# Optimization experiments

Measured on AMD Instinct MI355X. Metric: run time of the kernel, lower is better.

The kernel has to match this reference:

```python
import jax, jax.numpy as jnp
import numpy as np

B, T, D, H = 2, 1024, 1024, 16
DH = D // H
_PAIRS = [(0, 1), (0, 2), (0, 3), (1, 2), (1, 3), (2, 3)]
_J6 = jnp.array([[0, 0, 0, 0, 0, 1],
                 [0, 0, 0, 0, -1, 0],
                 [0, 0, 0, 1, 0, 0],
                 [0, 0, 1, 0, 0, 0],
                 [0, -1, 0, 0, 0, 0],
                 [1, 0, 0, 0, 0, 0]], dtype=jnp.float32)


def exterior(p1, p2):
    # Plucker coordinates of the line through 4-vectors p1, p2, L2-normalized.
    parts = [p1[..., i] * p2[..., j] - p1[..., j] * p2[..., i] for i, j in _PAIRS]
    L = jnp.stack(parts, axis=-1)  # (..., 6)
    n = jnp.maximum(jnp.linalg.norm(L, axis=-1, keepdims=True), 1e-12)
    return L / n


def setup_inputs() -> dict:
    key = jax.random.key(0)
    ks = jax.random.split(key, 10)
    s = 0.02
    return {
        "x": jax.random.normal(ks[0], (B, T, D), jnp.float32),
        "Wqkv": jax.random.normal(ks[1], (3 * D, D), jnp.float32) * s,
        "bqkv": jnp.zeros((3 * D,), jnp.float32),
        "W1w": jax.random.normal(ks[2], (4 * H, D), jnp.float32) * s,
        "W2w": jax.random.normal(ks[3], (4 * H, D), jnp.float32) * s,
        "W1r": jax.random.normal(ks[4], (4 * H, D), jnp.float32) * s,
        "W2r": jax.random.normal(ks[5], (4 * H, D), jnp.float32) * s,
        "bias_scale": jnp.full((H,), 0.1, jnp.float32),
        "Wout": jax.random.normal(ks[6], (D, D), jnp.float32) * s,
        "bout": jnp.zeros((D,), jnp.float32),
    }


def reference(x, Wqkv, bqkv, W1w, W2w, W1r, W2r, bias_scale, Wout, bout):
    Bb, Tt, Dd = x.shape
    scale = DH ** (-0.5)
    qkv = (x @ Wqkv.T + bqkv).reshape(Bb, Tt, 3, H, DH)
    q = jnp.transpose(qkv[:, :, 0], (0, 2, 1, 3))  # (B,H,T,dh)
    k = jnp.transpose(qkv[:, :, 1], (0, 2, 1, 3))
    v = jnp.transpose(qkv[:, :, 2], (0, 2, 1, 3))
    std_logits = jnp.einsum('bhtd,bhsd->bhts', q, k) * scale

    x_prev = jnp.concatenate([jnp.zeros((Bb, 1, Dd), x.dtype), x[:, :-1]], axis=1)
    w1 = (x_prev @ W1w.T).reshape(Bb, Tt, H, 4)
    w2 = (x @ W2w.T).reshape(Bb, Tt, H, 4)
    write_lines = exterior(w1, w2)  # (B,T,H,6)
    r1 = (x @ W1r.T).reshape(Bb, Tt, H, 4)
    r2 = (x @ W2r.T).reshape(Bb, Tt, H, 4)
    read_lines = exterior(r1, r2)  # (B,T,H,6)

    Jw = jnp.einsum('bthi,ij->bhtj', write_lines, _J6)  # (B,H,T,6)
    rd = jnp.transpose(read_lines, (0, 2, 1, 3))        # (B,H,T,6)

    outer = Jw[..., :, None] * Jw[..., None, :]          # (B,H,T,6,6)
    M_causal = jnp.cumsum(outer, axis=2)                 # running Gram state
    rd_M = jnp.einsum('bhti,bhtij->bhtj', rd, M_causal)  # (B,H,T,6)
    bias_raw = jnp.einsum('bhti,bhsi->bhts', rd_M, Jw)   # (B,H,T,T)
    bias = jnp.abs(bias_raw) * bias_scale.reshape(1, H, 1, 1)

    logits = std_logits + bias
    mask = jnp.triu(jnp.ones((Tt, Tt), bool), 1)
    logits = jnp.where(mask, -jnp.inf, logits)
    attn = jax.nn.softmax(logits, axis=-1)
    out = jnp.einsum('bhts,bhsd->bthd', attn, v).reshape(Bb, Tt, Dd)
    return out @ Wout.T + bout
```

## Files before the change

kernel.cpp:

```cpp
#include <hip/hip_runtime.h>
#include <math.h>

#define B_ 2
#define T_ 1024
#define D_ 1024
#define H_ 16
#define NA_ 3328

typedef __attribute__((ext_vector_type(8))) short bf16x8;
typedef __attribute__((ext_vector_type(4))) float f32x4;

__device__ inline unsigned short f2bf(float x) {
  return (unsigned short)((__float_as_uint(x) + 0x8000u) >> 16);
}
__device__ inline unsigned bfpack(float lo, float hi) {
  unsigned a = __float_as_uint(hi) + 0x8000u;
  unsigned b = __float_as_uint(lo) + 0x8000u;
  return __builtin_amdgcn_perm(a, b, 0x07060302);
}
__device__ inline void hl_split(float x, unsigned short& h, unsigned short& l) {
  unsigned short hh = f2bf(x);
  float hf = __uint_as_float(((unsigned)hh) << 16);
  l = f2bf(x - hf);
  h = hh;
}


#define GEMM_PROLOGUE_VARS()                                                   \
  const int tid = threadIdx.x;                                                 \
  const int w = tid >> 6, lane = tid & 63;                                     \
  const int lr = lane & 15, g = lane >> 4;                                     \
  const int wm = (w >> 1) * 64, wn = (w & 1) * 64;                             \
  const int row = tid >> 1, half = tid & 1;                                    \
  const int sw = (row & 3) << 4;                                               \
  const int by0 = (half * 32) ^ sw, by1 = (half * 32 + 16) ^ sw;

#define GEMM_STORE(bufA, bufB, a, b)                                           \
  {                                                                            \
    uint4 lo = make_uint4(bfpack(a[0].x, a[0].y), bfpack(a[0].z, a[0].w),      \
                          bfpack(a[1].x, a[1].y), bfpack(a[1].z, a[1].w));     \
    uint4 hi = make_uint4(bfpack(a[2].x, a[2].y), bfpack(a[2].z, a[2].w),      \
                          bfpack(a[3].x, a[3].y), bfpack(a[3].z, a[3].w));     \
    *(uint4*)(bufA + row * 64 + by0) = lo;                                     \
    *(uint4*)(bufA + row * 64 + by1) = hi;                                     \
    lo = make_uint4(bfpack(b[0].x, b[0].y), bfpack(b[0].z, b[0].w),            \
                    bfpack(b[1].x, b[1].y), bfpack(b[1].z, b[1].w));           \
    hi = make_uint4(bfpack(b[2].x, b[2].y), bfpack(b[2].z, b[2].w),            \
                    bfpack(b[3].x, b[3].y), bfpack(b[3].z, b[3].w));           \
    *(uint4*)(bufB + row * 64 + by0) = lo;                                     \
    *(uint4*)(bufB + row * 64 + by1) = hi;                                     \
  }

#define GEMM_COMPUTE(bufA, bufB)                                               \
  {                                                                            \
    bf16x8 af[4], bfr[4];                                                      \
    _Pragma("unroll") for (int i = 0; i < 4; ++i) {                            \
      const int rr = wm + i * 16 + lr;                                         \
      af[i] = *(const bf16x8*)(bufA + rr * 64 + ((g * 16) ^ ((rr & 3) << 4))); \
    }                                                                          \
    _Pragma("unroll") for (int i = 0; i < 4; ++i) {                            \
      const int rr = wn + i * 16 + lr;                                         \
      bfr[i] = *(const bf16x8*)(bufB + rr * 64 + ((g * 16) ^ ((rr & 3) << 4)));\
    }                                                                          \
    _Pragma("unroll") for (int i = 0; i < 4; ++i)                              \
    _Pragma("unroll") for (int j = 0; j < 4; ++j)                              \
      acc[i][j] = __builtin_amdgcn_mfma_f32_16x16x32_bf16(af[i], bfr[j],       \
                                                          acc[i][j], 0, 0, 0); \
  }

#define GEMM_LOAD(dst, base, slab)                                             \
  _Pragma("unroll") for (int i = 0; i < 4; ++i)                                \
      dst[i] = *(const float4*)(base + (slab) * 32 + i * 4);

__global__ __launch_bounds__(256) void gemm_qkv(
    const float* __restrict__ A, const float* __restrict__ Wqkv,
    const float* __restrict__ bqkv,
    const float* __restrict__ W1w, const float* __restrict__ W2w,
    const float* __restrict__ W1r, const float* __restrict__ W2r,
    float* __restrict__ C)
{
  __shared__ __align__(16) unsigned char As[2 * 8192];
  __shared__ __align__(16) unsigned char Bs[2 * 8192];
  const int m0 = blockIdx.y * 128, n0 = blockIdx.x * 128;
  GEMM_PROLOGUE_VARS();

  const float* Ap = A + (size_t)(m0 + row) * D_ + half * 16;
  const float* Bp;
  {
    const int cg = n0 + row;
    if (cg < 3072) Bp = Wqkv + (size_t)cg * D_;
    else {
      const int r = cg - 3072;
      const float* Wm = (r < 64) ? W1w : (r < 128) ? W2w : (r < 192) ? W1r : W2r;
      Bp = Wm + (size_t)(r & 63) * D_;
    }
    Bp += half * 16;
  }

  f32x4 acc[4][4];
  const f32x4 zf = {0.f, 0.f, 0.f, 0.f};
#pragma unroll
  for (int i = 0; i < 4; ++i)
#pragma unroll
    for (int j = 0; j < 4; ++j) acc[i][j] = zf;

  float4 aA[4], bA[4], aB[4], bB[4];
  GEMM_LOAD(aA, Ap, 0); GEMM_LOAD(bA, Bp, 0);
  GEMM_STORE(As, Bs, aA, bA);
  GEMM_LOAD(aB, Ap, 1); GEMM_LOAD(bB, Bp, 1);
  __syncthreads();

#pragma unroll 1
  for (int s = 0; s < 32; s += 2) {
    GEMM_COMPUTE(As, Bs);
    GEMM_STORE((As + 8192), (Bs + 8192), aB, bB);
    if (s + 2 < 32) { GEMM_LOAD(aA, Ap, s + 2); GEMM_LOAD(bA, Bp, s + 2); }
    __syncthreads();
    GEMM_COMPUTE((As + 8192), (Bs + 8192));
    if (s + 2 < 32) GEMM_STORE(As, Bs, aA, bA);
    if (s + 3 < 32) { GEMM_LOAD(aB, Ap, s + 3); GEMM_LOAD(bB, Bp, s + 3); }
    __syncthreads();
  }

#pragma unroll
  for (int i = 0; i < 4; ++i) {
    const int rbase = m0 + wm + i * 16 + 4 * g;
#pragma unroll
    for (int j = 0; j < 4; ++j) {
      const int col = n0 + wn + j * 16 + lr;
      const float bb = (col < 3072) ? bqkv[col] : 0.f;
#pragma unroll
      for (int r = 0; r < 4; ++r)
        C[(size_t)(rbase + r) * NA_ + col] = acc[i][j][r] + bb;
    }
  }
}

__global__ __launch_bounds__(256) void gemm_out(
    const float* __restrict__ A, const float* __restrict__ Bm,
    const float* __restrict__ bias, float* __restrict__ C)
{
  __shared__ __align__(16) unsigned char As[2 * 8192];
  __shared__ __align__(16) unsigned char Bs[2 * 8192];
  const int m0 = blockIdx.y * 128, n0 = blockIdx.x * 128;
  GEMM_PROLOGUE_VARS();

  const float* Ap = A + (size_t)(m0 + row) * D_ + half * 16;
  const float* Bp = Bm + (size_t)(n0 + row) * D_ + half * 16;

  f32x4 acc[4][4];
  const f32x4 zf = {0.f, 0.f, 0.f, 0.f};
#pragma unroll
  for (int i = 0; i < 4; ++i)
#pragma unroll
    for (int j = 0; j < 4; ++j) acc[i][j] = zf;

  float4 aA[4], bA[4], aB[4], bB[4];
  GEMM_LOAD(aA, Ap, 0); GEMM_LOAD(bA, Bp, 0);
  GEMM_STORE(As, Bs, aA, bA);
  GEMM_LOAD(aB, Ap, 1); GEMM_LOAD(bB, Bp, 1);
  __syncthreads();

#pragma unroll 1
  for (int s = 0; s < 32; s += 2) {
    GEMM_COMPUTE(As, Bs);
    GEMM_STORE((As + 8192), (Bs + 8192), aB, bB);
    if (s + 2 < 32) { GEMM_LOAD(aA, Ap, s + 2); GEMM_LOAD(bA, Bp, s + 2); }
    __syncthreads();
    GEMM_COMPUTE((As + 8192), (Bs + 8192));
    if (s + 2 < 32) GEMM_STORE(As, Bs, aA, bA);
    if (s + 3 < 32) { GEMM_LOAD(aB, Ap, s + 3); GEMM_LOAD(bB, Bp, s + 3); }
    __syncthreads();
  }

#pragma unroll
  for (int i = 0; i < 4; ++i) {
    const int rbase = m0 + wm + i * 16 + 4 * g;
#pragma unroll
    for (int j = 0; j < 4; ++j) {
      const int col = n0 + wn + j * 16 + lr;
      const float bb = bias[col];
#pragma unroll
      for (int r = 0; r < 4; ++r)
        C[(size_t)(rbase + r) * D_ + col] = acc[i][j][r] + bb;
    }
  }
}

__global__ __launch_bounds__(256) void exterior_kernel(
    const float* __restrict__ qkvp,
    float* __restrict__ Jw, float* __restrict__ rd,
    unsigned* __restrict__ Jwpk)
{
  const int i = blockIdx.x * 256 + threadIdx.x;
  const int h = i & 15;
  const int t = (i >> 4) & 1023;
  const int b = i >> 14;
  const size_t rowt = ((size_t)(b * T_) + t) * NA_;

  float4 p1w = make_float4(0.f, 0.f, 0.f, 0.f);
  if (t > 0) p1w = *(const float4*)(qkvp + rowt - NA_ + 3072 + h * 4);
  const float4 p2w = *(const float4*)(qkvp + rowt + 3136 + h * 4);
  const float4 p1r = *(const float4*)(qkvp + rowt + 3200 + h * 4);
  const float4 p2r = *(const float4*)(qkvp + rowt + 3264 + h * 4);

  const size_t base = ((size_t)(b * H_ + h) * T_ + t) * 6;
  {
    const float L0 = p1w.x * p2w.y - p1w.y * p2w.x;
    const float L1 = p1w.x * p2w.z - p1w.z * p2w.x;
    const float L2 = p1w.x * p2w.w - p1w.w * p2w.x;
    const float L3 = p1w.y * p2w.z - p1w.z * p2w.y;
    const float L4 = p1w.y * p2w.w - p1w.w * p2w.y;
    const float L5 = p1w.z * p2w.w - p1w.w * p2w.z;
    const float n = sqrtf(L0 * L0 + L1 * L1 + L2 * L2 + L3 * L3 + L4 * L4 + L5 * L5);
    const float inv = 1.f / fmaxf(n, 1e-12f);
    float jv[6] = {L5 * inv, -L4 * inv, L3 * inv, L2 * inv, -L1 * inv, L0 * inv};
#pragma unroll
    for (int k = 0; k < 6; ++k) Jw[base + k] = jv[k];
    unsigned short JH[6], JL[6];
#pragma unroll
    for (int k = 0; k < 6; ++k) hl_split(jv[k], JH[k], JL[k]);
    unsigned* jp = Jwpk + (((size_t)(b * H_ + h) * T_ + t) << 4);
    unsigned h01 = JH[0] | ((unsigned)JH[1] << 16);
    unsigned h23 = JH[2] | ((unsigned)JH[3] << 16);
    unsigned h45 = JH[4] | ((unsigned)JH[5] << 16);
    jp[0] = h01; jp[1] = h23; jp[2] = h45;
    jp[3] = JL[0] | ((unsigned)JL[1] << 16);
    jp[4] = JL[2] | ((unsigned)JL[3] << 16);
    jp[5] = JL[4] | ((unsigned)JL[5] << 16);
    jp[6] = h01; jp[7] = h23; jp[8] = h45;
#pragma unroll
    for (int k = 9; k < 16; ++k) jp[k] = 0;
  }
  {
    const float L0 = p1r.x * p2r.y - p1r.y * p2r.x;
    const float L1 = p1r.x * p2r.z - p1r.z * p2r.x;
    const float L2 = p1r.x * p2r.w - p1r.w * p2r.x;
    const float L3 = p1r.y * p2r.z - p1r.z * p2r.y;
    const float L4 = p1r.y * p2r.w - p1r.w * p2r.y;
    const float L5 = p1r.z * p2r.w - p1r.w * p2r.z;
    const float n = sqrtf(L0 * L0 + L1 * L1 + L2 * L2 + L3 * L3 + L4 * L4 + L5 * L5);
    const float inv = 1.f / fmaxf(n, 1e-12f);
    rd[base + 0] = L0 * inv;
    rd[base + 1] = L1 * inv;
    rd[base + 2] = L2 * inv;
    rd[base + 3] = L3 * inv;
    rd[base + 4] = L4 * inv;
    rd[base + 5] = L5 * inv;
  }
}

__global__ __launch_bounds__(256) void scan_kernel(
    const float* __restrict__ Jw, const float* __restrict__ rd,
    unsigned* __restrict__ rdMpk)
{
  __shared__ float sc[256][36];
  const int tid = threadIdx.x;
  const int bh = blockIdx.x;
  const float* Jb = Jw + (size_t)bh * T_ * 6;
  const float* Rb = rd + (size_t)bh * T_ * 6;
  const int t0 = tid * 4;

  float M[36];
#pragma unroll
  for (int i = 0; i < 36; ++i) M[i] = 0.f;
  for (int tt = 0; tt < 4; ++tt) {
    float j6[6];
#pragma unroll
    for (int i = 0; i < 6; ++i) j6[i] = Jb[(size_t)(t0 + tt) * 6 + i];
#pragma unroll
    for (int a = 0; a < 6; ++a)
#pragma unroll
      for (int c = 0; c < 6; ++c)
        M[a * 6 + c] = fmaf(j6[a], j6[c], M[a * 6 + c]);
  }
#pragma unroll
  for (int i = 0; i < 36; ++i) sc[tid][i] = M[i];
  __syncthreads();

  float Mp[36];
#pragma unroll
  for (int i = 0; i < 36; ++i) Mp[i] = 0.f;
  for (int j = 0; j < tid; ++j) {
#pragma unroll
    for (int i = 0; i < 36; ++i) Mp[i] += sc[j][i];
  }

  for (int tt = 0; tt < 4; ++tt) {
    const int t = t0 + tt;
    float j6[6], r6[6];
#pragma unroll
    for (int i = 0; i < 6; ++i) { j6[i] = Jb[(size_t)t * 6 + i]; r6[i] = Rb[(size_t)t * 6 + i]; }
#pragma unroll
    for (int a = 0; a < 6; ++a)
#pragma unroll
      for (int c = 0; c < 6; ++c)
        Mp[a * 6 + c] = fmaf(j6[a], j6[c], Mp[a * 6 + c]);
    float s6[6];
#pragma unroll
    for (int jj = 0; jj < 6; ++jj) {
      float s = 0.f;
#pragma unroll
      for (int a = 0; a < 6; ++a) s = fmaf(r6[a], Mp[a * 6 + jj], s);
      s6[jj] = s;
    }
    unsigned short hh[6], ll[6];
#pragma unroll
    for (int i = 0; i < 6; ++i) hl_split(s6[i], hh[i], ll[i]);
    unsigned* ob = rdMpk + (((size_t)bh * T_ + t) << 4);
    unsigned h01 = hh[0] | ((unsigned)hh[1] << 16);
    unsigned h23 = hh[2] | ((unsigned)hh[3] << 16);
    unsigned h45 = hh[4] | ((unsigned)hh[5] << 16);
    ob[0] = h01; ob[1] = h23; ob[2] = h45;
    ob[3] = h01; ob[4] = h23; ob[5] = h45;
    ob[6] = ll[0] | ((unsigned)ll[1] << 16);
    ob[7] = ll[2] | ((unsigned)ll[3] << 16);
    ob[8] = ll[4] | ((unsigned)ll[5] << 16);
#pragma unroll
    for (int i = 9; i < 16; ++i) ob[i] = 0;
  }
}

__global__ __launch_bounds__(256) void attn_mfma(
    const float* __restrict__ qkv,
    const unsigned* __restrict__ Jwpk,
    const unsigned* __restrict__ rdMpk,
    const float* __restrict__ bias_scale,
    float* __restrict__ attnout)
{
  __shared__ __align__(16) unsigned char smem[31744];
  unsigned char* KT = smem;
  unsigned char* VT = smem + 9216;
  unsigned*      JW = (unsigned*)(smem + 18432);
  unsigned char* PB = smem + 22528;

  const int gid = blockIdx.x;
  const int bh = gid & 31;
  const int c = (gid < 256) ? (15 - (gid >> 5)) : ((gid - 256) >> 5);
  const int b = bh >> 4, h = bh & 15;
  const int tid = threadIdx.x;
  const int w = tid >> 6;
  const int lane = tid & 63;
  const int lr = lane & 15;
  const int g = lane >> 4;
  const int t0 = c * 64;
  const int nT = c + 1;

  const size_t qkvbase = ((size_t)b * T_) * NA_ + h * 64;
  const size_t jb = (size_t)(b * H_ + h) * T_;

  int srow[4], scol[4];
#pragma unroll
  for (int p = 0; p < 4; ++p) {
    const int idx = p * 256 + tid;
    srow[p] = idx >> 4;
    scol[p] = (idx & 15) * 4;
  }

#pragma unroll
  for (int p = 0; p < 4; ++p) {
    const float4 v = *(const float4*)(qkv + qkvbase + (size_t)(t0 + srow[p]) * NA_ + scol[p]);
    const unsigned d0 = bfpack(v.x * 0.125f, v.y * 0.125f);
    const unsigned d1 = bfpack(v.z * 0.125f, v.w * 0.125f);
    const int byte = srow[p] * 144 + ((scol[p] * 2) ^ ((srow[p] & 7) << 4));
    *(uint2*)(KT + byte) = make_uint2(d0, d1);
  }
  __syncthreads();
  bf16x8 qa[2];
  {
    const int qrow = w * 16 + lr;
#pragma unroll
    for (int kb = 0; kb < 2; ++kb) {
      const int byte = qrow * 144 + (((kb * 64) + 16 * g) ^ ((qrow & 7) << 4));
      qa[kb] = *(const bf16x8*)(KT + byte);
    }
  }
  bf16x8 ra;
  {
    const int t = t0 + w * 16 + lr;
    ra = *(const bf16x8*)(rdMpk + ((jb + t) << 4) + g * 4);
  }
  const float bsc = bias_scale[h];
  __syncthreads();

  float m[4], lsum[4];
  f32x4 O[4];
  const f32x4 zf = {0.f, 0.f, 0.f, 0.f};
#pragma unroll
  for (int r = 0; r < 4; ++r) { m[r] = -1e30f; lsum[r] = 0.f; }
#pragma unroll
  for (int d = 0; d < 4; ++d) O[d] = zf;

  float4 kreg[4], vreg[4];
  uint4 jreg;
  const int jrow = tid >> 2, jpart = (tid & 3) * 4;
  {
#pragma unroll
    for (int p = 0; p < 4; ++p) {
      const size_t rb = qkvbase + (size_t)srow[p] * NA_ + scol[p];
      kreg[p] = *(const float4*)(qkv + rb + 1024);
      vreg[p] = *(const float4*)(qkv + rb + 2048);
    }
    jreg = *(const uint4*)(Jwpk + ((jb + jrow) << 4) + jpart);
  }

  for (int ti = 0; ti < nT; ++ti) {
    const int s0 = ti * 64;
    __syncthreads();
#pragma unroll
    for (int p = 0; p < 4; ++p) {
      const unsigned d0 = bfpack(kreg[p].x, kreg[p].y);
      const unsigned d1 = bfpack(kreg[p].z, kreg[p].w);
      const int byte = srow[p] * 144 + ((scol[p] * 2) ^ ((srow[p] & 7) << 4));
      *(uint2*)(KT + byte) = make_uint2(d0, d1);
      const int s = srow[p];
#pragma unroll
      for (int i = 0; i < 4; ++i) {
        const int d = scol[p] + i;
        const float vv = (i == 0) ? vreg[p].x : (i == 1) ? vreg[p].y : (i == 2) ? vreg[p].z : vreg[p].w;
        const int vbyte = d * 144 + ((2 * s) ^ ((d & 7) << 4));
        *(unsigned short*)(VT + vbyte) = f2bf(vv);
      }
    }
    *(uint4*)(JW + jrow * 16 + jpart) = jreg;
    __syncthreads();
    if (ti + 1 < nT) {
      const int s0n = s0 + 64;
#pragma unroll
      for (int p = 0; p < 4; ++p) {
        const size_t rb = qkvbase + (size_t)(s0n + srow[p]) * NA_ + scol[p];
        kreg[p] = *(const float4*)(qkv + rb + 1024);
        vreg[p] = *(const float4*)(qkv + rb + 2048);
      }
      jreg = *(const uint4*)(Jwpk + ((jb + s0n + jrow) << 4) + jpart);
    }

    f32x4 S[4], Sb[4];
#pragma unroll
    for (int cb = 0; cb < 4; ++cb) {
      const int srw = cb * 16 + lr;
      f32x4 a = zf;
#pragma unroll
      for (int kb = 0; kb < 2; ++kb) {
        const int byte = srw * 144 + (((kb * 64) + 16 * g) ^ ((srw & 7) << 4));
        const bf16x8 kf = *(const bf16x8*)(KT + byte);
        a = __builtin_amdgcn_mfma_f32_16x16x32_bf16(qa[kb], kf, a, 0, 0, 0);
      }
      S[cb] = a;
      union { uint4 u; bf16x8 v; } tmp;
      tmp.u = *(const uint4*)(JW + srw * 16 + g * 4);
      Sb[cb] = __builtin_amdgcn_mfma_f32_16x16x32_bf16(ra, tmp.v, zf, 0, 0, 0);
    }

    const bool diag = (s0 == t0);
    float logit[4][4];
#pragma unroll
    for (int cb = 0; cb < 4; ++cb) {
#pragma unroll
      for (int r = 0; r < 4; ++r) {
        float lg = S[cb][r] + fabsf(Sb[cb][r]) * bsc;
        if (diag && (cb * 16 + lr > w * 16 + 4 * g + r)) lg = -1e30f;
        logit[cb][r] = lg;
      }
    }
#pragma unroll
    for (int r = 0; r < 4; ++r) {
      float mx = fmaxf(fmaxf(logit[0][r], logit[1][r]), fmaxf(logit[2][r], logit[3][r]));
      mx = fmaxf(mx, __shfl_xor(mx, 1));
      mx = fmaxf(mx, __shfl_xor(mx, 2));
      mx = fmaxf(mx, __shfl_xor(mx, 4));
      mx = fmaxf(mx, __shfl_xor(mx, 8));
      const float nm = fmaxf(m[r], mx);
      const float sc = __expf(m[r] - nm);
      m[r] = nm;
      lsum[r] *= sc;
#pragma unroll
      for (int d = 0; d < 4; ++d) O[d][r] *= sc;
    }
#pragma unroll
    for (int cb = 0; cb < 4; ++cb) {
#pragma unroll
      for (int r = 0; r < 4; ++r) {
        const float p = __expf(logit[cb][r] - m[r]);
        lsum[r] += p;
        const int q = 4 * g + r;
        const int s = cb * 16 + lr;
        const int byte = w * 2304 + q * 144 + ((2 * s) ^ ((q & 7) << 4));
        *(unsigned short*)(PB + byte) = f2bf(p);
      }
    }
    asm volatile("s_waitcnt lgkmcnt(0)" ::: "memory");
    __builtin_amdgcn_sched_barrier(0);

    bf16x8 pa[2];
#pragma unroll
    for (int kb = 0; kb < 2; ++kb) {
      const int byte = w * 2304 + lr * 144 + (((kb * 64) + 16 * g) ^ ((lr & 7) << 4));
      pa[kb] = *(const bf16x8*)(PB + byte);
    }
#pragma unroll
    for (int db = 0; db < 4; ++db) {
#pragma unroll
      for (int kb = 0; kb < 2; ++kb) {
        const int d = db * 16 + lr;
        const int byte = d * 144 + (((kb * 64) + 16 * g) ^ ((d & 7) << 4));
        const bf16x8 vf = *(const bf16x8*)(VT + byte);
        O[db] = __builtin_amdgcn_mfma_f32_16x16x32_bf16(pa[kb], vf, O[db], 0, 0, 0);
      }
    }
  }

#pragma unroll
  for (int r = 0; r < 4; ++r) {
    float l = lsum[r];
    l += __shfl_xor(l, 1);
    l += __shfl_xor(l, 2);
    l += __shfl_xor(l, 4);
    l += __shfl_xor(l, 8);
    lsum[r] = 1.f / l;
  }
  {
    const int qb = w * 16 + 4 * g;
#pragma unroll
    for (int db = 0; db < 4; ++db) {
#pragma unroll
      for (int r = 0; r < 4; ++r) {
        const int t = t0 + qb + r;
        attnout[((size_t)(b * T_ + t)) * 1024 + h * 64 + db * 16 + lr] = O[db][r] * lsum[r];
      }
    }
  }
}

extern "C" void kernel_launch(void* const* d_in, const int* in_sizes, int n_in,
                              void* d_out, int out_size, void* d_ws, size_t ws_size,
                              hipStream_t stream)
{
  (void)in_sizes; (void)n_in; (void)out_size; (void)ws_size;
  const float* x    = (const float*)d_in[0];
  const float* Wqkv = (const float*)d_in[1];
  const float* bqkv = (const float*)d_in[2];
  const float* W1w  = (const float*)d_in[3];
  const float* W2w  = (const float*)d_in[4];
  const float* W1r  = (const float*)d_in[5];
  const float* W2r  = (const float*)d_in[6];
  const float* bsc  = (const float*)d_in[7];
  const float* Wout = (const float*)d_in[8];
  const float* bout = (const float*)d_in[9];
  float* out = (float*)d_out;

  float*    qkvp    = (float*)d_ws;
  float*    Jw      = qkvp + (size_t)B_ * T_ * NA_;
  float*    rd      = Jw + (size_t)B_ * H_ * T_ * 6;
  unsigned* Jwpk    = (unsigned*)(rd + (size_t)B_ * H_ * T_ * 6);
  unsigned* rdMpk   = Jwpk + ((size_t)B_ * H_ * T_ << 4);
  float*    attnout = (float*)(rdMpk + ((size_t)B_ * H_ * T_ << 4));

  gemm_qkv<<<dim3(NA_ / 128, B_ * T_ / 128), 256, 0, stream>>>(
      x, Wqkv, bqkv, W1w, W2w, W1r, W2r, qkvp);
  exterior_kernel<<<dim3(B_ * T_ * H_ / 256), 256, 0, stream>>>(
      qkvp, Jw, rd, Jwpk);
  scan_kernel<<<dim3(B_ * H_), 256, 0, stream>>>(Jw, rd, rdMpk);
  attn_mfma<<<dim3(B_ * H_ * (T_ / 64)), 256, 0, stream>>>(
      qkvp, Jwpk, rdMpk, bsc, attnout);
  gemm_out<<<dim3(D_ / 128, B_ * T_ / 128), 256, 0, stream>>>(
      attnout, Wout, bout, out);
}
```

Measured before the change: 139.9 us.

## Pre-convert inputs to bf16, store QKV and attention output in bf16, parallel scan

Adds a kernel that converts x and all weight matrices to bf16 once, so the GEMMs load bf16 tiles directly instead of converting fp32 in the inner loop. The GEMMs switch to 128x64 tiles with 128 threads and a swizzled block order. QKV and the attention output are now written as bf16, and the projection lines go to a separate fp32 buffer. The attention kernel reads Q and K fragments straight from global bf16 and double-buffers a transposed V tile. The scan kernel replaces its serial prefix loop with a Hillis-Steele scan in shared memory. Per-call weight conversion adds extra traffic, and keeping intermediates in bf16 lowers precision.

```diff
diff --git a/kernel.cpp b/kernel.cpp
--- a/kernel.cpp
+++ b/kernel.cpp
@@ -5,7 +5,6 @@
 #define T_ 1024
 #define D_ 1024
 #define H_ 16
-#define NA_ 3328
 
 typedef __attribute__((ext_vector_type(8))) short bf16x8;
 typedef __attribute__((ext_vector_type(4))) float f32x4;
@@ -25,170 +24,164 @@
   h = hh;
 }
 
-
-#define GEMM_PROLOGUE_VARS()                                                   \
+#define CN1 2097152
+#define CN2 3407872
+#define CN3 1048576
+__global__ __launch_bounds__(256) void convert_kernel(
+    const float* __restrict__ x, const float* __restrict__ Wqkv,
+    const float* __restrict__ W1w, const float* __restrict__ W2w,
+    const float* __restrict__ W1r, const float* __restrict__ W2r,
+    const float* __restrict__ Wout,
+    unsigned short* __restrict__ xb, unsigned short* __restrict__ Wb,
+    unsigned short* __restrict__ Woutb)
+{
+  const long i8 = ((long)blockIdx.x * 256 + threadIdx.x) * 8;
+  const float* src;
+  unsigned short* dst;
+  if (i8 < CN1) {
+    src = x + i8; dst = xb + i8;
+  } else if (i8 < CN1 + CN2) {
+    const long j = i8 - CN1;
+    const int row = (int)(j >> 10), col = (int)(j & 1023);
+    if (row < 3072) src = Wqkv + (size_t)row * 1024 + col;
+    else {
+      const int r = row - 3072;
+      const float* Wm = (r < 64) ? W1w : (r < 128) ? W2w : (r < 192) ? W1r : W2r;
+      src = Wm + (size_t)(r & 63) * 1024 + col;
+    }
+    dst = Wb + j;
+  } else {
+    const long j = i8 - CN1 - CN2;
+    src = Wout + j; dst = Woutb + j;
+  }
+  const float4 v0 = *(const float4*)src;
+  const float4 v1 = *(const float4*)(src + 4);
+  uint4 o;
+  o.x = bfpack(v0.x, v0.y); o.y = bfpack(v0.z, v0.w);
+  o.z = bfpack(v1.x, v1.y); o.w = bfpack(v1.z, v1.w);
+  *(uint4*)dst = o;
+}
+
+#define G_PRO()                                                                \
   const int tid = threadIdx.x;                                                 \
   const int w = tid >> 6, lane = tid & 63;                                     \
   const int lr = lane & 15, g = lane >> 4;                                     \
-  const int wm = (w >> 1) * 64, wn = (w & 1) * 64;                             \
-  const int row = tid >> 1, half = tid & 1;                                    \
-  const int sw = (row & 3) << 4;                                               \
-  const int by0 = (half * 32) ^ sw, by1 = (half * 32 + 16) ^ sw;
-
-#define GEMM_STORE(bufA, bufB, a, b)                                           \
-  {                                                                            \
-    uint4 lo = make_uint4(bfpack(a[0].x, a[0].y), bfpack(a[0].z, a[0].w),      \
-                          bfpack(a[1].x, a[1].y), bfpack(a[1].z, a[1].w));     \
-    uint4 hi = make_uint4(bfpack(a[2].x, a[2].y), bfpack(a[2].z, a[2].w),      \
-                          bfpack(a[3].x, a[3].y), bfpack(a[3].z, a[3].w));     \
-    *(uint4*)(bufA + row * 64 + by0) = lo;                                     \
-    *(uint4*)(bufA + row * 64 + by1) = hi;                                     \
-    lo = make_uint4(bfpack(b[0].x, b[0].y), bfpack(b[0].z, b[0].w),            \
-                    bfpack(b[1].x, b[1].y), bfpack(b[1].z, b[1].w));           \
-    hi = make_uint4(bfpack(b[2].x, b[2].y), bfpack(b[2].z, b[2].w),            \
-                    bfpack(b[3].x, b[3].y), bfpack(b[3].z, b[3].w));           \
-    *(uint4*)(bufB + row * 64 + by0) = lo;                                     \
-    *(uint4*)(bufB + row * 64 + by1) = hi;                                     \
-  }
-
-#define GEMM_COMPUTE(bufA, bufB)                                               \
-  {                                                                            \
-    bf16x8 af[4], bfr[4];                                                      \
-    _Pragma("unroll") for (int i = 0; i < 4; ++i) {                            \
-      const int rr = wm + i * 16 + lr;                                         \
-      af[i] = *(const bf16x8*)(bufA + rr * 64 + ((g * 16) ^ ((rr & 3) << 4))); \
-    }                                                                          \
-    _Pragma("unroll") for (int i = 0; i < 4; ++i) {                            \
-      const int rr = wn + i * 16 + lr;                                         \
-      bfr[i] = *(const bf16x8*)(bufB + rr * 64 + ((g * 16) ^ ((rr & 3) << 4)));\
-    }                                                                          \
-    _Pragma("unroll") for (int i = 0; i < 4; ++i)                              \
-    _Pragma("unroll") for (int j = 0; j < 4; ++j)                              \
-      acc[i][j] = __builtin_amdgcn_mfma_f32_16x16x32_bf16(af[i], bfr[j],       \
-                                                          acc[i][j], 0, 0, 0); \
-  }
-
-#define GEMM_LOAD(dst, base, slab)                                             \
+  const int wm = w * 64;                                                       \
+  const int brow = tid & 63, bhalf = tid >> 6;
+
+#define G_LOADA(d, s) {                                                        \
+  d[0] = *(const uint4*)(Ap + (s) * 32);                                       \
+  d[1] = *(const uint4*)(Ap + (s) * 32 + 8);                                   \
+  d[2] = *(const uint4*)(Ap + (s) * 32 + 16);                                  \
+  d[3] = *(const uint4*)(Ap + (s) * 32 + 24); }
+#define G_LOADB(d, s) {                                                        \
+  d[0] = *(const uint4*)(Bp + (s) * 32);                                       \
+  d[1] = *(const uint4*)(Bp + (s) * 32 + 8); }
+#define G_STORE(bi, a, b) {                                                    \
+  unsigned char* SA_ = As + (bi) * 8192;                                       \
+  *(uint4*)(SA_ + 0 * 2048 + tid * 16) = a[0];                                 \
+  *(uint4*)(SA_ + 1 * 2048 + tid * 16) = a[1];                                 \
+  *(uint4*)(SA_ + 2 * 2048 + tid * 16) = a[2];                                 \
+  *(uint4*)(SA_ + 3 * 2048 + tid * 16) = a[3];                                 \
+  unsigned char* SB_ = Bs + (bi) * 4096;                                       \
+  *(uint4*)(SB_ + (2 * bhalf) * 1024 + brow * 16) = b[0];                      \
+  *(uint4*)(SB_ + (2 * bhalf + 1) * 1024 + brow * 16) = b[1]; }
+#define G_COMPUTE(bi) {                                                        \
+  const unsigned char* SA_ = As + (bi) * 8192;                                 \
+  const unsigned char* SB_ = Bs + (bi) * 4096;                                 \
+  bf16x8 af[4], bfr[4];                                                        \
   _Pragma("unroll") for (int i = 0; i < 4; ++i)                                \
-      dst[i] = *(const float4*)(base + (slab) * 32 + i * 4);
-
-__global__ __launch_bounds__(256) void gemm_qkv(
-    const float* __restrict__ A, const float* __restrict__ Wqkv,
+    af[i] = *(const bf16x8*)(SA_ + g * 2048 + (wm + i * 16 + lr) * 16);        \
+  _Pragma("unroll") for (int j = 0; j < 4; ++j)                                \
+    bfr[j] = *(const bf16x8*)(SB_ + g * 1024 + (j * 16 + lr) * 16);            \
+  _Pragma("unroll") for (int i = 0; i < 4; ++i)                                \
+  _Pragma("unroll") for (int j = 0; j < 4; ++j)                                \
+    acc[i][j] = __builtin_amdgcn_mfma_f32_16x16x32_bf16(af[i], bfr[j],         \
+                                                        acc[i][j], 0, 0, 0); }
+#define G_MAIN()                                                               \
+  f32x4 acc[4][4];                                                             \
+  const f32x4 zf = {0.f, 0.f, 0.f, 0.f};                                       \
+  _Pragma("unroll") for (int i = 0; i < 4; ++i)                                \
+  _Pragma("unroll") for (int j = 0; j < 4; ++j) acc[i][j] = zf;                \
+  uint4 a0[4], b0[2], a1[4], b1[2];                                            \
+  G_LOADA(a0, 0); G_LOADB(b0, 0);                                              \
+  G_STORE(0, a0, b0);                                                          \
+  G_LOADA(a1, 1); G_LOADB(b1, 1);                                              \
+  __syncthreads();                                                             \
+  _Pragma("unroll 1") for (int s = 0; s < 32; s += 2) {                        \
+    G_COMPUTE(0);                                                              \
+    G_STORE(1, a1, b1);                                                        \
+    if (s + 2 < 32) { G_LOADA(a0, s + 2); G_LOADB(b0, s + 2); }                \
+    __syncthreads();                                                           \
+    G_COMPUTE(1);                                                              \
+    if (s + 2 < 32) G_STORE(0, a0, b0);                                        \
+    if (s + 3 < 32) { G_LOADA(a1, s + 3); G_LOADB(b1, s + 3); }                \
+    __syncthreads();                                                           \
+  }
+
+__global__ __launch_bounds__(128) void gemm_qkv(
+    const unsigned short* __restrict__ Ab, const unsigned short* __restrict__ Bb,
     const float* __restrict__ bqkv,
-    const float* __restrict__ W1w, const float* __restrict__ W2w,
-    const float* __restrict__ W1r, const float* __restrict__ W2r,
-    float* __restrict__ C)
+    unsigned short* __restrict__ Cq, float* __restrict__ Clines)
 {
   __shared__ __align__(16) unsigned char As[2 * 8192];
-  __shared__ __align__(16) unsigned char Bs[2 * 8192];
-  const int m0 = blockIdx.y * 128, n0 = blockIdx.x * 128;
-  GEMM_PROLOGUE_VARS();
-
-  const float* Ap = A + (size_t)(m0 + row) * D_ + half * 16;
-  const float* Bp;
-  {
-    const int cg = n0 + row;
-    if (cg < 3072) Bp = Wqkv + (size_t)cg * D_;
-    else {
-      const int r = cg - 3072;
-      const float* Wm = (r < 64) ? W1w : (r < 128) ? W2w : (r < 192) ? W1r : W2r;
-      Bp = Wm + (size_t)(r & 63) * D_;
-    }
-    Bp += half * 16;
-  }
-
-  f32x4 acc[4][4];
-  const f32x4 zf = {0.f, 0.f, 0.f, 0.f};
-#pragma unroll
-  for (int i = 0; i < 4; ++i)
-#pragma unroll
-    for (int j = 0; j < 4; ++j) acc[i][j] = zf;
-
-  float4 aA[4], bA[4], aB[4], bB[4];
-  GEMM_LOAD(aA, Ap, 0); GEMM_LOAD(bA, Bp, 0);
-  GEMM_STORE(As, Bs, aA, bA);
-  GEMM_LOAD(aB, Ap, 1); GEMM_LOAD(bB, Bp, 1);
-  __syncthreads();
-
-#pragma unroll 1
-  for (int s = 0; s < 32; s += 2) {
-    GEMM_COMPUTE(As, Bs);
-    GEMM_STORE((As + 8192), (Bs + 8192), aB, bB);
-    if (s + 2 < 32) { GEMM_LOAD(aA, Ap, s + 2); GEMM_LOAD(bA, Bp, s + 2); }
-    __syncthreads();
-    GEMM_COMPUTE((As + 8192), (Bs + 8192));
-    if (s + 2 < 32) GEMM_STORE(As, Bs, aA, bA);
-    if (s + 3 < 32) { GEMM_LOAD(aB, Ap, s + 3); GEMM_LOAD(bB, Bp, s + 3); }
-    __syncthreads();
-  }
-
+  __shared__ __align__(16) unsigned char Bs[2 * 4096];
+  const int bid = blockIdx.x;
+  const int sid = (bid & 7) * 104 + (bid >> 3);
+  const int m0 = (sid & 15) * 128, n0 = (sid >> 4) * 64;
+  G_PRO();
+  const unsigned short* Ap = Ab + (size_t)(m0 + tid) * 1024;
+  const unsigned short* Bp = Bb + (size_t)(n0 + brow) * 1024 + bhalf * 16;
+  G_MAIN();
 #pragma unroll
   for (int i = 0; i < 4; ++i) {
     const int rbase = m0 + wm + i * 16 + 4 * g;
 #pragma unroll
     for (int j = 0; j < 4; ++j) {
-      const int col = n0 + wn + j * 16 + lr;
-      const float bb = (col < 3072) ? bqkv[col] : 0.f;
-#pragma unroll
-      for (int r = 0; r < 4; ++r)
-        C[(size_t)(rbase + r) * NA_ + col] = acc[i][j][r] + bb;
-    }
-  }
-}
-
-__global__ __launch_bounds__(256) void gemm_out(
-    const float* __restrict__ A, const float* __restrict__ Bm,
+      const int col = n0 + j * 16 + lr;
+      if (col < 3072) {
+        const float bb = bqkv[col];
+#pragma unroll
+        for (int r = 0; r < 4; ++r)
+          Cq[(size_t)(rbase + r) * 3072 + col] = f2bf(acc[i][j][r] + bb);
+      } else {
+#pragma unroll
+        for (int r = 0; r < 4; ++r)
+          Clines[(size_t)(rbase + r) * 256 + col - 3072] = acc[i][j][r];
+      }
+    }
+  }
+}
+
+__global__ __launch_bounds__(128) void gemm_out(
+    const unsigned short* __restrict__ Ab, const unsigned short* __restrict__ Bb,
     const float* __restrict__ bias, float* __restrict__ C)
 {
   __shared__ __align__(16) unsigned char As[2 * 8192];
-  __shared__ __align__(16) unsigned char Bs[2 * 8192];
-  const int m0 = blockIdx.y * 128, n0 = blockIdx.x * 128;
-  GEMM_PROLOGUE_VARS();
-
-  const float* Ap = A + (size_t)(m0 + row) * D_ + half * 16;
-  const float* Bp = Bm + (size_t)(n0 + row) * D_ + half * 16;
-
-  f32x4 acc[4][4];
-  const f32x4 zf = {0.f, 0.f, 0.f, 0.f};
-#pragma unroll
-  for (int i = 0; i < 4; ++i)
-#pragma unroll
-    for (int j = 0; j < 4; ++j) acc[i][j] = zf;
-
-  float4 aA[4], bA[4], aB[4], bB[4];
-  GEMM_LOAD(aA, Ap, 0); GEMM_LOAD(bA, Bp, 0);
-  GEMM_STORE(As, Bs, aA, bA);
-  GEMM_LOAD(aB, Ap, 1); GEMM_LOAD(bB, Bp, 1);
-  __syncthreads();
-
-#pragma unroll 1
-  for (int s = 0; s < 32; s += 2) {
-    GEMM_COMPUTE(As, Bs);
-    GEMM_STORE((As + 8192), (Bs + 8192), aB, bB);
-    if (s + 2 < 32) { GEMM_LOAD(aA, Ap, s + 2); GEMM_LOAD(bA, Bp, s + 2); }
-    __syncthreads();
-    GEMM_COMPUTE((As + 8192), (Bs + 8192));
-    if (s + 2 < 32) GEMM_STORE(As, Bs, aA, bA);
-    if (s + 3 < 32) { GEMM_LOAD(aB, Ap, s + 3); GEMM_LOAD(bB, Bp, s + 3); }
-    __syncthreads();
-  }
-
+  __shared__ __align__(16) unsigned char Bs[2 * 4096];
+  const int bid = blockIdx.x;
+  const int sid = (bid & 7) * 32 + (bid >> 3);
+  const int m0 = (sid & 15) * 128, n0 = (sid >> 4) * 64;
+  G_PRO();
+  const unsigned short* Ap = Ab + (size_t)(m0 + tid) * 1024;
+  const unsigned short* Bp = Bb + (size_t)(n0 + brow) * 1024 + bhalf * 16;
+  G_MAIN();
 #pragma unroll
   for (int i = 0; i < 4; ++i) {
     const int rbase = m0 + wm + i * 16 + 4 * g;
 #pragma unroll
     for (int j = 0; j < 4; ++j) {
-      const int col = n0 + wn + j * 16 + lr;
+      const int col = n0 + j * 16 + lr;
       const float bb = bias[col];
 #pragma unroll
       for (int r = 0; r < 4; ++r)
-        C[(size_t)(rbase + r) * D_ + col] = acc[i][j][r] + bb;
+        C[(size_t)(rbase + r) * 1024 + col] = acc[i][j][r] + bb;
     }
   }
 }
 
 __global__ __launch_bounds__(256) void exterior_kernel(
-    const float* __restrict__ qkvp,
+    const float* __restrict__ linesf,
     float* __restrict__ Jw, float* __restrict__ rd,
     unsigned* __restrict__ Jwpk)
 {
@@ -196,13 +189,13 @@
   const int h = i & 15;
   const int t = (i >> 4) & 1023;
   const int b = i >> 14;
-  const size_t rowt = ((size_t)(b * T_) + t) * NA_;
+  const size_t rowt = ((size_t)(b * T_) + t) * 256;
 
   float4 p1w = make_float4(0.f, 0.f, 0.f, 0.f);
-  if (t > 0) p1w = *(const float4*)(qkvp + rowt - NA_ + 3072 + h * 4);
-  const float4 p2w = *(const float4*)(qkvp + rowt + 3136 + h * 4);
-  const float4 p1r = *(const float4*)(qkvp + rowt + 3200 + h * 4);
-  const float4 p2r = *(const float4*)(qkvp + rowt + 3264 + h * 4);
+  if (t > 0) p1w = *(const float4*)(linesf + rowt - 256 + h * 4);
+  const float4 p2w = *(const float4*)(linesf + rowt + 64 + h * 4);
+  const float4 p1r = *(const float4*)(linesf + rowt + 128 + h * 4);
+  const float4 p2r = *(const float4*)(linesf + rowt + 192 + h * 4);
 
   const size_t base = ((size_t)(b * H_ + h) * T_ + t) * 6;
   {
@@ -254,16 +247,16 @@
     const float* __restrict__ Jw, const float* __restrict__ rd,
     unsigned* __restrict__ rdMpk)
 {
-  __shared__ float sc[256][36];
+  __shared__ float sc[256][40];
   const int tid = threadIdx.x;
   const int bh = blockIdx.x;
   const float* Jb = Jw + (size_t)bh * T_ * 6;
   const float* Rb = rd + (size_t)bh * T_ * 6;
   const int t0 = tid * 4;
 
-  float M[36];
-#pragma unroll
-  for (int i = 0; i < 36; ++i) M[i] = 0.f;
+  float L[36], M[36];
+#pragma unroll
+  for (int i = 0; i < 36; ++i) L[i] = 0.f;
   for (int tt = 0; tt < 4; ++tt) {
     float j6[6];
 #pragma unroll
@@ -272,19 +265,39 @@
     for (int a = 0; a < 6; ++a)
 #pragma unroll
       for (int c = 0; c < 6; ++c)
-        M[a * 6 + c] = fmaf(j6[a], j6[c], M[a * 6 + c]);
-  }
-#pragma unroll
-  for (int i = 0; i < 36; ++i) sc[tid][i] = M[i];
+        L[a * 6 + c] = fmaf(j6[a], j6[c], L[a * 6 + c]);
+  }
+#pragma unroll
+  for (int i = 0; i < 36; ++i) M[i] = L[i];
+#pragma unroll
+  for (int k = 0; k < 9; ++k)
+    *(float4*)&sc[tid][k * 4] = make_float4(M[k*4], M[k*4+1], M[k*4+2], M[k*4+3]);
   __syncthreads();
 
+  for (int off = 1; off < 256; off <<= 1) {
+    float4 tmp[9];
+    const bool act = (tid >= off);
+    if (act) {
+#pragma unroll
+      for (int k = 0; k < 9; ++k) tmp[k] = *(const float4*)&sc[tid - off][k * 4];
+    }
+    __syncthreads();
+    if (act) {
+#pragma unroll
+      for (int k = 0; k < 9; ++k) {
+        M[k*4]   += tmp[k].x; M[k*4+1] += tmp[k].y;
+        M[k*4+2] += tmp[k].z; M[k*4+3] += tmp[k].w;
+      }
+#pragma unroll
+      for (int k = 0; k < 9; ++k)
+        *(float4*)&sc[tid][k * 4] = make_float4(M[k*4], M[k*4+1], M[k*4+2], M[k*4+3]);
+    }
+    __syncthreads();
+  }
+
   float Mp[36];
 #pragma unroll
-  for (int i = 0; i < 36; ++i) Mp[i] = 0.f;
-  for (int j = 0; j < tid; ++j) {
-#pragma unroll
-    for (int i = 0; i < 36; ++i) Mp[i] += sc[j][i];
-  }
+  for (int i = 0; i < 36; ++i) Mp[i] = M[i] - L[i];
 
   for (int tt = 0; tt < 4; ++tt) {
     const int t = t0 + tt;
@@ -322,17 +335,15 @@
 }
 
 __global__ __launch_bounds__(256) void attn_mfma(
-    const float* __restrict__ qkv,
+    const unsigned short* __restrict__ qkvb,
     const unsigned* __restrict__ Jwpk,
     const unsigned* __restrict__ rdMpk,
     const float* __restrict__ bias_scale,
-    float* __restrict__ attnout)
-{
-  __shared__ __align__(16) unsigned char smem[31744];
-  unsigned char* KT = smem;
-  unsigned char* VT = smem + 9216;
-  unsigned*      JW = (unsigned*)(smem + 18432);
-  unsigned char* PB = smem + 22528;
+    unsigned short* __restrict__ attnb)
+{
+  __shared__ __align__(16) unsigned char smem[24576];
+  unsigned char* VT = smem;
+  unsigned char* PB = smem + 16384;
 
   const int gid = blockIdx.x;
   const int bh = gid & 31;
@@ -346,42 +357,20 @@
   const int t0 = c * 64;
   const int nT = c + 1;
 
-  const size_t qkvbase = ((size_t)b * T_) * NA_ + h * 64;
+  const unsigned short* Qb = qkvb + (size_t)b * T_ * 3072 + h * 64;
+  const unsigned short* Kb = Qb + 1024;
+  const unsigned short* Vb = Qb + 2048;
   const size_t jb = (size_t)(b * H_ + h) * T_;
 
-  int srow[4], scol[4];
-#pragma unroll
-  for (int p = 0; p < 4; ++p) {
-    const int idx = p * 256 + tid;
-    srow[p] = idx >> 4;
-    scol[p] = (idx & 15) * 4;
-  }
-
-#pragma unroll
-  for (int p = 0; p < 4; ++p) {
-    const float4 v = *(const float4*)(qkv + qkvbase + (size_t)(t0 + srow[p]) * NA_ + scol[p]);
-    const unsigned d0 = bfpack(v.x * 0.125f, v.y * 0.125f);
-    const unsigned d1 = bfpack(v.z * 0.125f, v.w * 0.125f);
-    const int byte = srow[p] * 144 + ((scol[p] * 2) ^ ((srow[p] & 7) << 4));
-    *(uint2*)(KT + byte) = make_uint2(d0, d1);
-  }
-  __syncthreads();
   bf16x8 qa[2];
   {
-    const int qrow = w * 16 + lr;
-#pragma unroll
-    for (int kb = 0; kb < 2; ++kb) {
-      const int byte = qrow * 144 + (((kb * 64) + 16 * g) ^ ((qrow & 7) << 4));
-      qa[kb] = *(const bf16x8*)(KT + byte);
-    }
-  }
-  bf16x8 ra;
-  {
-    const int t = t0 + w * 16 + lr;
-    ra = *(const bf16x8*)(rdMpk + ((jb + t) << 4) + g * 4);
-  }
+    const size_t qr = (size_t)(t0 + w * 16 + lr) * 3072;
+#pragma unroll
+    for (int kb = 0; kb < 2; ++kb)
+      qa[kb] = *(const bf16x8*)(Qb + qr + kb * 32 + g * 8);
+  }
+  bf16x8 ra = *(const bf16x8*)(rdMpk + ((jb + t0 + w * 16 + lr) << 4) + g * 4);
   const float bsc = bias_scale[h];
-  __syncthreads();
 
   float m[4], lsum[4];
   f32x4 O[4];
@@ -391,65 +380,49 @@
 #pragma unroll
   for (int d = 0; d < 4; ++d) O[d] = zf;
 
-  float4 kreg[4], vreg[4];
-  uint4 jreg;
-  const int jrow = tid >> 2, jpart = (tid & 3) * 4;
+  const int sp = tid & 31, d8 = tid >> 5;
+  uint4 v0, v1, v0n, v1n;
   {
-#pragma unroll
-    for (int p = 0; p < 4; ++p) {
-      const size_t rb = qkvbase + (size_t)srow[p] * NA_ + scol[p];
-      kreg[p] = *(const float4*)(qkv + rb + 1024);
-      vreg[p] = *(const float4*)(qkv + rb + 2048);
-    }
-    jreg = *(const uint4*)(Jwpk + ((jb + jrow) << 4) + jpart);
+    const size_t r0 = (size_t)(2 * sp) * 3072 + d8 * 8;
+    v0 = *(const uint4*)(Vb + r0);
+    v1 = *(const uint4*)(Vb + r0 + 3072);
   }
 
   for (int ti = 0; ti < nT; ++ti) {
     const int s0 = ti * 64;
+    {
+      unsigned* vt = (unsigned*)(VT + (ti & 1) * 8192);
+      const unsigned a[4] = {v0.x, v0.y, v0.z, v0.w};
+      const unsigned bq[4] = {v1.x, v1.y, v1.z, v1.w};
+#pragma unroll
+      for (int i = 0; i < 8; ++i) {
+        const int d = d8 * 8 + i;
+        const unsigned dw = (i & 1)
+            ? __builtin_amdgcn_perm(bq[i >> 1], a[i >> 1], 0x07060302)
+            : __builtin_amdgcn_perm(bq[i >> 1], a[i >> 1], 0x05040100);
+        vt[d * 32 + (sp ^ ((d & 7) << 2))] = dw;
+      }
+    }
+    if (ti + 1 < nT) {
+      const size_t rn = (size_t)(s0 + 64 + 2 * sp) * 3072 + d8 * 8;
+      v0n = *(const uint4*)(Vb + rn);
+      v1n = *(const uint4*)(Vb + rn + 3072);
+    }
     __syncthreads();
-#pragma unroll
-    for (int p = 0; p < 4; ++p) {
-      const unsigned d0 = bfpack(kreg[p].x, kreg[p].y);
-      const unsigned d1 = bfpack(kreg[p].z, kreg[p].w);
-      const int byte = srow[p] * 144 + ((scol[p] * 2) ^ ((srow[p] & 7) << 4));
-      *(uint2*)(KT + byte) = make_uint2(d0, d1);
-      const int s = srow[p];
-#pragma unroll
-      for (int i = 0; i < 4; ++i) {
-        const int d = scol[p] + i;
-        const float vv = (i == 0) ? vreg[p].x : (i == 1) ? vreg[p].y : (i == 2) ? vreg[p].z : vreg[p].w;
-        const int vbyte = d * 144 + ((2 * s) ^ ((d & 7) << 4));
-        *(unsigned short*)(VT + vbyte) = f2bf(vv);
-      }
-    }
-    *(uint4*)(JW + jrow * 16 + jpart) = jreg;
-    __syncthreads();
-    if (ti + 1 < nT) {
-      const int s0n = s0 + 64;
-#pragma unroll
-      for (int p = 0; p < 4; ++p) {
-        const size_t rb = qkvbase + (size_t)(s0n + srow[p]) * NA_ + scol[p];
-        kreg[p] = *(const float4*)(qkv + rb + 1024);
-        vreg[p] = *(const float4*)(qkv + rb + 2048);
-      }
-      jreg = *(const uint4*)(Jwpk + ((jb + s0n + jrow) << 4) + jpart);
-    }
 
     f32x4 S[4], Sb[4];
 #pragma unroll
     for (int cb = 0; cb < 4; ++cb) {
-      const int srw = cb * 16 + lr;
+      const size_t srow = (size_t)(s0 + cb * 16 + lr);
       f32x4 a = zf;
 #pragma unroll
       for (int kb = 0; kb < 2; ++kb) {
-        const int byte = srw * 144 + (((kb * 64) + 16 * g) ^ ((srw & 7) << 4));
-        const bf16x8 kf = *(const bf16x8*)(KT + byte);
+        const bf16x8 kf = *(const bf16x8*)(Kb + srow * 3072 + kb * 32 + g * 8);
         a = __builtin_amdgcn_mfma_f32_16x16x32_bf16(qa[kb], kf, a, 0, 0, 0);
       }
       S[cb] = a;
-      union { uint4 u; bf16x8 v; } tmp;
-      tmp.u = *(const uint4*)(JW + srw * 16 + g * 4);
-      Sb[cb] = __builtin_amdgcn_mfma_f32_16x16x32_bf16(ra, tmp.v, zf, 0, 0, 0);
+      const bf16x8 jw = *(const bf16x8*)(Jwpk + ((jb + srow) << 4) + g * 4);
+      Sb[cb] = __builtin_amdgcn_mfma_f32_16x16x32_bf16(ra, jw, zf, 0, 0, 0);
     }
 
     const bool diag = (s0 == t0);
@@ -458,7 +431,7 @@
     for (int cb = 0; cb < 4; ++cb) {
 #pragma unroll
       for (int r = 0; r < 4; ++r) {
-        float lg = S[cb][r] + fabsf(Sb[cb][r]) * bsc;
+        float lg = S[cb][r] * 0.125f + fabsf(Sb[cb][r]) * bsc;
         if (diag && (cb * 16 + lr > w * 16 + 4 * g + r)) lg = -1e30f;
         logit[cb][r] = lg;
       }
@@ -485,7 +458,7 @@
         lsum[r] += p;
         const int q = 4 * g + r;
         const int s = cb * 16 + lr;
-        const int byte = w * 2304 + q * 144 + ((2 * s) ^ ((q & 7) << 4));
+        const int byte = w * 2048 + q * 128 + ((2 * s) ^ ((q & 7) << 4));
         *(unsigned short*)(PB + byte) = f2bf(p);
       }
     }
@@ -495,19 +468,21 @@
     bf16x8 pa[2];
 #pragma unroll
     for (int kb = 0; kb < 2; ++kb) {
-      const int byte = w * 2304 + lr * 144 + (((kb * 64) + 16 * g) ^ ((lr & 7) << 4));
+      const int byte = w * 2048 + lr * 128 + (((kb * 64) + 16 * g) ^ ((lr & 7) << 4));
       pa[kb] = *(const bf16x8*)(PB + byte);
     }
+    const unsigned char* vtb = VT + (ti & 1) * 8192;
 #pragma unroll
     for (int db = 0; db < 4; ++db) {
+      const int d = db * 16 + lr;
 #pragma unroll
       for (int kb = 0; kb < 2; ++kb) {
-        const int d = db * 16 + lr;
-        const int byte = d * 144 + (((kb * 64) + 16 * g) ^ ((d & 7) << 4));
-        const bf16x8 vf = *(const bf16x8*)(VT + byte);
+        const int byte = d * 128 + (((kb * 64) + 16 * g) ^ ((d & 7) << 4));
+        const bf16x8 vf = *(const bf16x8*)(vtb + byte);
         O[db] = __builtin_amdgcn_mfma_f32_16x16x32_bf16(pa[kb], vf, O[db], 0, 0, 0);
       }
     }
+    v0 = v0n; v1 = v1n;
   }
 
 #pragma unroll
@@ -526,7 +501,8 @@
 #pragma unroll
       for (int r = 0; r < 4; ++r) {
         const int t = t0 + qb + r;
-        attnout[((size_t)(b * T_ + t)) * 1024 + h * 64 + db * 16 + lr] = O[db][r] * lsum[r];
+        attnb[(size_t)(b * T_ + t) * 1024 + h * 64 + db * 16 + lr] =
+            f2bf(O[db][r] * lsum[r]);
       }
     }
   }
@@ -549,20 +525,24 @@
   const float* bout = (const float*)d_in[9];
   float* out = (float*)d_out;
 
-  float*    qkvp    = (float*)d_ws;
-  float*    Jw      = qkvp + (size_t)B_ * T_ * NA_;
-  float*    rd      = Jw + (size_t)B_ * H_ * T_ * 6;
-  unsigned* Jwpk    = (unsigned*)(rd + (size_t)B_ * H_ * T_ * 6);
-  unsigned* rdMpk   = Jwpk + ((size_t)B_ * H_ * T_ << 4);
-  float*    attnout = (float*)(rdMpk + ((size_t)B_ * H_ * T_ << 4));
-
-  gemm_qkv<<<dim3(NA_ / 128, B_ * T_ / 128), 256, 0, stream>>>(
-      x, Wqkv, bqkv, W1w, W2w, W1r, W2r, qkvp);
+  unsigned short* xb    = (unsigned short*)d_ws;
+  unsigned short* Wb    = xb + (size_t)2048 * 1024;
+  unsigned short* Woutb = Wb + (size_t)3328 * 1024;
+  unsigned short* qkvb  = Woutb + (size_t)1024 * 1024;
+  unsigned short* attnb = qkvb + (size_t)2048 * 3072;
+  float* linesf = (float*)(attnb + (size_t)2048 * 1024);
+  float* Jw     = linesf + (size_t)2048 * 256;
+  float* rd     = Jw + 196608;
+  unsigned* Jwpk  = (unsigned*)(rd + 196608);
+  unsigned* rdMpk = Jwpk + 524288;
+
+  convert_kernel<<<dim3(3200), 256, 0, stream>>>(
+      x, Wqkv, W1w, W2w, W1r, W2r, Wout, xb, Wb, Woutb);
+  gemm_qkv<<<dim3(832), 128, 0, stream>>>(xb, Wb, bqkv, qkvb, linesf);
   exterior_kernel<<<dim3(B_ * T_ * H_ / 256), 256, 0, stream>>>(
-      qkvp, Jw, rd, Jwpk);
+      linesf, Jw, rd, Jwpk);
   scan_kernel<<<dim3(B_ * H_), 256, 0, stream>>>(Jw, rd, rdMpk);
   attn_mfma<<<dim3(B_ * H_ * (T_ / 64)), 256, 0, stream>>>(
-      qkvp, Jwpk, rdMpk, bsc, attnout);
-  gemm_out<<<dim3(D_ / 128, B_ * T_ / 128), 256, 0, stream>>>(
-      attnout, Wout, bout, out);
-}
+      qkvb, Jwpk, rdMpk, bsc, attnb);
+  gemm_out<<<dim3(256), 128, 0, stream>>>(attnb, Woutb, bout, out);
+}
```

Result: slower. 260.2 us (+85.9%).
